# Kernel optimization log

Hardware: AMD Instinct MI355X
Metric: run time of the kernel (lower is better)

## Reference

```python
import jax, jax.numpy as jnp
import numpy as np

N_NODES = 100000
N_EDGES = 1600000
IN_F = 256
OUT_F = 128


def setup_inputs() -> dict:
    key = jax.random.key(0)
    k1, k2, k3, k4, k5, k6 = jax.random.split(key, 6)
    init_range = float(np.sqrt(6.0 / (IN_F + OUT_F)))
    stdv = 1.0 / float(np.sqrt(OUT_F))
    return {
        "x": jax.random.normal(k1, (N_NODES, IN_F), dtype=jnp.float32),
        "weight": jax.random.uniform(k2, (IN_F, OUT_F), dtype=jnp.float32, minval=-init_range, maxval=init_range),
        "bias": jax.random.uniform(k3, (OUT_F,), dtype=jnp.float32, minval=-stdv, maxval=stdv),
        "adj_val": jax.random.uniform(k4, (N_EDGES,), dtype=jnp.float32),
        "adj_row": jax.random.randint(k5, (N_EDGES,), 0, N_NODES),  # destination node per edge
        "adj_col": jax.random.randint(k6, (N_EDGES,), 0, N_NODES),  # source node per edge
    }


def reference(x, weight, bias, adj_val, adj_row, adj_col):
    # support = X @ W   (dense GEMM, [N, in] x [in, out])
    support = x @ weight
    # output = spmm(adj, support): gather source rows, scale by edge value,
    # segment-sum into destination rows. Honors COO sparsity; no [N,N] dense.
    gathered = support[adj_col] * adj_val[:, None]          # [E, out]
    out = jax.ops.segment_sum(gathered, adj_row, num_segments=N_NODES)
    return out + bias
```

## Files before the change

kernel.cpp:

```cpp
#include <hip/hip_runtime.h>

#define N_NODES 100000
#define N_EDGES 1600000
#define IN_F 256
#define OUT_F 128

#define NBUCK 1563
#define FBUCK 64
#define CAP 1664

#define SORT_CHUNKS 128
#define CHUNK_E (N_EDGES / SORT_CHUNKS)

#define GEMM_BM 128
#define GEMM_BLOCKS ((N_NODES + GEMM_BM - 1) / GEMM_BM)

typedef __attribute__((ext_vector_type(8))) short bf16x8;
typedef __attribute__((ext_vector_type(4))) float f32x4;

__device__ __forceinline__ unsigned short f2bf(float f) {
    unsigned u = __float_as_uint(f);
    unsigned r = u + 0x7fffu + ((u >> 16) & 1u);
    return (unsigned short)(r >> 16);
}

__global__ __launch_bounds__(256) void wz_kernel(const float* __restrict__ w,
                                                 unsigned short* __restrict__ wt,
                                                 int* __restrict__ cursor) {
    const int tid = threadIdx.x;
    if (blockIdx.x < 128) {
        int c = blockIdx.x;
        wt[c * IN_F + tid] = f2bf(w[tid * OUT_F + c]);
    } else {
        int i = (blockIdx.x - 128) * 256 + tid;
        if (i < NBUCK) cursor[i] = 0;
    }
}

__global__ __launch_bounds__(512, 4) void gemm_sort_kernel(const float* __restrict__ x,
                                                           const unsigned short* __restrict__ wt,
                                                           unsigned short* __restrict__ support,
                                                           const int* __restrict__ rowi,
                                                           const int* __restrict__ coli,
                                                           const float* __restrict__ val,
                                                           int* __restrict__ cursor,
                                                           uint2* __restrict__ tmp) {
    __shared__ unsigned short ws[128 * 256];
    __shared__ int bh[NBUCK];

    const int tid = threadIdx.x;

    if (blockIdx.x < SORT_CHUNKS) {
        const int c = blockIdx.x;
        for (int i = tid; i < NBUCK; i += 512) bh[i] = 0;
        __syncthreads();
        const int e0 = c * CHUNK_E;
        for (int i = tid; i < CHUNK_E; i += 512)
            atomicAdd(&bh[rowi[e0 + i] >> 6], 1);
        __syncthreads();
        for (int i = tid; i < NBUCK; i += 512) {
            int n = bh[i];
            bh[i] = n ? atomicAdd(&cursor[i], n) : 0;
        }
        __syncthreads();
        for (int i = tid; i < CHUNK_E; i += 512) {
            int e = e0 + i;
            int dst = rowi[e];
            int b = dst >> 6;
            int pos = atomicAdd(&bh[b], 1);
            tmp[(size_t)b * CAP + pos] =
                make_uint2(((unsigned)(dst & 63) << 17) | (unsigned)coli[e],
                           __float_as_uint(val[e]));
        }
        return;
    }

    const int lane = tid & 63;
    const int wv = tid >> 6;
    const int row0 = (blockIdx.x - SORT_CHUNKS) * GEMM_BM;
    const int l15 = lane & 15;
    const int kq = lane >> 4;

#pragma unroll
    for (int it = 0; it < 8; ++it) {
        int ci = it * 512 + tid;
        int col = ci >> 5, ch = ci & 31;
        uint4 v = *reinterpret_cast<const uint4*>(&wt[col * IN_F + ch * 8]);
        int slot = ch ^ (col & 7);
        *reinterpret_cast<uint4*>(&ws[col * 256 + slot * 8]) = v;
    }
    __syncthreads();

    int arow = row0 + wv * 16 + l15;
    if (arow > N_NODES - 1) arow = N_NODES - 1;
    const float* xrow = &x[(size_t)arow * IN_F + kq * 8];

    f32x4 acc[8];
#pragma unroll
    for (int n = 0; n < 8; ++n) acc[n] = (f32x4){0.f, 0.f, 0.f, 0.f};

#pragma unroll
    for (int kt = 0; kt < 8; ++kt) {
        f32x4 a0 = *reinterpret_cast<const f32x4*>(xrow + kt * 32);
        f32x4 a1 = *reinterpret_cast<const f32x4*>(xrow + kt * 32 + 4);
        bf16x8 af;
        af[0] = (short)f2bf(a0[0]); af[1] = (short)f2bf(a0[1]);
        af[2] = (short)f2bf(a0[2]); af[3] = (short)f2bf(a0[3]);
        af[4] = (short)f2bf(a1[0]); af[5] = (short)f2bf(a1[1]);
        af[6] = (short)f2bf(a1[2]); af[7] = (short)f2bf(a1[3]);
#pragma unroll
        for (int n = 0; n < 8; ++n) {
            int col = n * 16 + l15;
            int slot = (kt * 4 + kq) ^ (col & 7);
            bf16x8 bfv = *reinterpret_cast<const bf16x8*>(&ws[col * 256 + slot * 8]);
            acc[n] = __builtin_amdgcn_mfma_f32_16x16x32_bf16(af, bfv, acc[n], 0, 0, 0);
        }
    }

#pragma unroll
    for (int r = 0; r < 4; ++r) {
        int row = row0 + wv * 16 + kq * 4 + r;
        if (row < N_NODES) {
#pragma unroll
            for (int n = 0; n < 8; ++n) {
                support[(size_t)row * OUT_F + n * 16 + l15] = f2bf(acc[n][r]);
            }
        }
    }
}

__global__ __launch_bounds__(256) void fine_accum_kernel(const unsigned short* __restrict__ support,
                                                         const uint2* __restrict__ tmp,
                                                         const int* __restrict__ cursor,
                                                         const float* __restrict__ bias,
                                                         float* __restrict__ out) {
    __shared__ uint2 plds[CAP];
    __shared__ int hist[FBUCK];
    __shared__ int scanb[FBUCK];
    __shared__ int cur[FBUCK];

    const int tid = threadIdx.x, b = blockIdx.x;
    const int cnt = cursor[b];
    const size_t base = (size_t)b * CAP;

    if (tid < FBUCK) hist[tid] = 0;
    __syncthreads();
    for (int i = tid; i < cnt; i += 256)
        atomicAdd(&hist[tmp[base + i].x >> 17], 1);
    __syncthreads();
    if (tid < FBUCK) scanb[tid] = hist[tid];
    __syncthreads();
#pragma unroll
    for (int off = 1; off < FBUCK; off <<= 1) {
        int t = (tid < FBUCK && tid >= off) ? scanb[tid - off] : 0;
        __syncthreads();
        if (tid < FBUCK) scanb[tid] += t;
        __syncthreads();
    }
    if (tid < FBUCK) cur[tid] = scanb[tid] - hist[tid];
    __syncthreads();
    for (int i = tid; i < cnt; i += 256) {
        uint2 u = tmp[base + i];
        int dl = u.x >> 17;
        int pos = atomicAdd(&cur[dl], 1);
        plds[pos] = make_uint2(u.x & 0x1FFFFu, u.y);
    }
    __syncthreads();

    const int lane = tid & 63;
    const int wv = tid >> 6;
    const int grp = lane >> 4;
    const int l16 = lane & 15;

    float4 b0 = *reinterpret_cast<const float4*>(&bias[l16 * 8]);
    float4 b1 = *reinterpret_cast<const float4*>(&bias[l16 * 8 + 4]);

    for (int ni = 0; ni < 16; ++ni) {
        const int dl = wv * 16 + ni;
        const int node = b * FBUCK + dl;
        if (node >= N_NODES) break;
        const int s = (dl == 0) ? 0 : scanb[dl - 1];
        const int e = scanb[dl];

        float acc[8];
#pragma unroll
        for (int t = 0; t < 8; ++t) acc[t] = 0.f;

        int j = s + grp;
        for (; j + 4 < e; j += 8) {
            uint2 p0 = plds[j];
            uint2 p1 = plds[j + 4];
            uint4 s0 = *reinterpret_cast<const uint4*>(&support[(size_t)p0.x * OUT_F + l16 * 8]);
            uint4 s1 = *reinterpret_cast<const uint4*>(&support[(size_t)p1.x * OUT_F + l16 * 8]);
            float v0 = __uint_as_float(p0.y);
            float v1 = __uint_as_float(p1.y);
            unsigned u0[4] = {s0.x, s0.y, s0.z, s0.w};
            unsigned u1[4] = {s1.x, s1.y, s1.z, s1.w};
#pragma unroll
            for (int q = 0; q < 4; ++q) {
                acc[2 * q + 0] += __uint_as_float(u0[q] << 16) * v0;
                acc[2 * q + 1] += __uint_as_float(u0[q] & 0xffff0000u) * v0;
                acc[2 * q + 0] += __uint_as_float(u1[q] << 16) * v1;
                acc[2 * q + 1] += __uint_as_float(u1[q] & 0xffff0000u) * v1;
            }
        }
        for (; j < e; j += 4) {
            uint2 p0 = plds[j];
            uint4 s0 = *reinterpret_cast<const uint4*>(&support[(size_t)p0.x * OUT_F + l16 * 8]);
            float v0 = __uint_as_float(p0.y);
            unsigned u0[4] = {s0.x, s0.y, s0.z, s0.w};
#pragma unroll
            for (int q = 0; q < 4; ++q) {
                acc[2 * q + 0] += __uint_as_float(u0[q] << 16) * v0;
                acc[2 * q + 1] += __uint_as_float(u0[q] & 0xffff0000u) * v0;
            }
        }

#pragma unroll
        for (int t = 0; t < 8; ++t) {
            acc[t] += __shfl_xor(acc[t], 16);
            acc[t] += __shfl_xor(acc[t], 32);
        }

        if (grp == 0) {
            f32x4 o0 = {acc[0] + b0.x, acc[1] + b0.y, acc[2] + b0.z, acc[3] + b0.w};
            f32x4 o1 = {acc[4] + b1.x, acc[5] + b1.y, acc[6] + b1.z, acc[7] + b1.w};
            f32x4* op = reinterpret_cast<f32x4*>(&out[(size_t)node * OUT_F + l16 * 8]);
            __builtin_nontemporal_store(o0, op);
            __builtin_nontemporal_store(o1, op + 1);
        }
    }
}

extern "C" void kernel_launch(void* const* d_in, const int* in_sizes, int n_in,
                              void* d_out, int out_size, void* d_ws, size_t ws_size,
                              hipStream_t stream) {
    const float* x       = (const float*)d_in[0];
    const float* weight  = (const float*)d_in[1];
    const float* bias    = (const float*)d_in[2];
    const float* adj_val = (const float*)d_in[3];
    const int*   adj_row = (const int*)d_in[4];
    const int*   adj_col = (const int*)d_in[5];
    float* out = (float*)d_out;

    unsigned short* support = (unsigned short*)d_ws;
    unsigned short* wt = support + (size_t)N_NODES * OUT_F;
    int* cursor = (int*)(wt + IN_F * OUT_F);
    uint2* tmp = (uint2*)(cursor + 1564);

    wz_kernel<<<128 + 7, 256, 0, stream>>>(weight, wt, cursor);
    gemm_sort_kernel<<<SORT_CHUNKS + GEMM_BLOCKS, 512, 0, stream>>>(
        x, wt, support, adj_row, adj_col, adj_val, cursor, tmp);
    fine_accum_kernel<<<NBUCK, 256, 0, stream>>>(support, tmp, cursor, bias, out);
}
```

Measured before the change: 116.1 us.

## Move edge bucket counting into the first kernel, scatter alongside GEMM

Splits the two-pass bucket sort across kernels. The histogram and the per-chunk bucket base reservation now run in the first kernel, together with the weight transpose, and write per-chunk bases to a workspace table. The GEMM kernel's sort blocks then only scatter edges, so the sort blocks sharing the GEMM launch are shorter and should not delay it. The sort chunk count also doubles to 256, and cursor zeroing moves to a memset. This costs an extra kernel/memset launch, a bases table of about 1.6 MB, and a second read of the row indices.

```diff
diff --git a/kernel.cpp b/kernel.cpp
--- a/kernel.cpp
+++ b/kernel.cpp
@@ -9,8 +9,8 @@
 #define FBUCK 64
 #define CAP 1664
 
-#define SORT_CHUNKS 128
-#define CHUNK_E (N_EDGES / SORT_CHUNKS)
+#define NCHUNK 256
+#define CHUNK_E (N_EDGES / NCHUNK)
 
 #define GEMM_BM 128
 #define GEMM_BLOCKS ((N_NODES + GEMM_BM - 1) / GEMM_BM)
@@ -24,50 +24,55 @@
     return (unsigned short)(r >> 16);
 }
 
-__global__ __launch_bounds__(256) void wz_kernel(const float* __restrict__ w,
-                                                 unsigned short* __restrict__ wt,
-                                                 int* __restrict__ cursor) {
+__global__ __launch_bounds__(256) void count_wtrans_kernel(const int* __restrict__ rowi,
+                                                           int* __restrict__ cursor,
+                                                           int* __restrict__ bases,
+                                                           const float* __restrict__ w,
+                                                           unsigned short* __restrict__ wt) {
     const int tid = threadIdx.x;
-    if (blockIdx.x < 128) {
-        int c = blockIdx.x;
+    if (blockIdx.x >= NCHUNK) {
+        int c = blockIdx.x - NCHUNK;
         wt[c * IN_F + tid] = f2bf(w[tid * OUT_F + c]);
-    } else {
-        int i = (blockIdx.x - 128) * 256 + tid;
-        if (i < NBUCK) cursor[i] = 0;
-    }
-}
-
-__global__ __launch_bounds__(512, 4) void gemm_sort_kernel(const float* __restrict__ x,
-                                                           const unsigned short* __restrict__ wt,
-                                                           unsigned short* __restrict__ support,
-                                                           const int* __restrict__ rowi,
-                                                           const int* __restrict__ coli,
-                                                           const float* __restrict__ val,
-                                                           int* __restrict__ cursor,
-                                                           uint2* __restrict__ tmp) {
+        return;
+    }
+    __shared__ int bh[NBUCK];
+    const int c = blockIdx.x;
+    for (int i = tid; i < NBUCK; i += 256) bh[i] = 0;
+    __syncthreads();
+    const int e0 = c * CHUNK_E;
+    for (int i = tid; i < CHUNK_E; i += 256)
+        atomicAdd(&bh[rowi[e0 + i] >> 6], 1);
+    __syncthreads();
+    for (int i = tid; i < NBUCK; i += 256) {
+        int n = bh[i];
+        bases[i * NCHUNK + c] = n ? atomicAdd(&cursor[i], n) : 0;
+    }
+}
+
+__global__ __launch_bounds__(512, 4) void gemm_scatter_kernel(const float* __restrict__ x,
+                                                              const unsigned short* __restrict__ wt,
+                                                              unsigned short* __restrict__ support,
+                                                              const int* __restrict__ rowi,
+                                                              const int* __restrict__ coli,
+                                                              const float* __restrict__ val,
+                                                              const int* __restrict__ bases,
+                                                              uint2* __restrict__ tmp) {
     __shared__ unsigned short ws[128 * 256];
-    __shared__ int bh[NBUCK];
+    __shared__ int cur[NBUCK];
 
     const int tid = threadIdx.x;
 
-    if (blockIdx.x < SORT_CHUNKS) {
+    if (blockIdx.x < NCHUNK) {
         const int c = blockIdx.x;
-        for (int i = tid; i < NBUCK; i += 512) bh[i] = 0;
+        for (int i = tid; i < NBUCK; i += 512)
+            cur[i] = bases[i * NCHUNK + c];
         __syncthreads();
         const int e0 = c * CHUNK_E;
-        for (int i = tid; i < CHUNK_E; i += 512)
-            atomicAdd(&bh[rowi[e0 + i] >> 6], 1);
-        __syncthreads();
-        for (int i = tid; i < NBUCK; i += 512) {
-            int n = bh[i];
-            bh[i] = n ? atomicAdd(&cursor[i], n) : 0;
-        }
-        __syncthreads();
         for (int i = tid; i < CHUNK_E; i += 512) {
             int e = e0 + i;
             int dst = rowi[e];
             int b = dst >> 6;
-            int pos = atomicAdd(&bh[b], 1);
+            int pos = atomicAdd(&cur[b], 1);
             tmp[(size_t)b * CAP + pos] =
                 make_uint2(((unsigned)(dst & 63) << 17) | (unsigned)coli[e],
                            __float_as_uint(val[e]));
@@ -77,7 +82,7 @@
 
     const int lane = tid & 63;
     const int wv = tid >> 6;
-    const int row0 = (blockIdx.x - SORT_CHUNKS) * GEMM_BM;
+    const int row0 = (blockIdx.x - NCHUNK) * GEMM_BM;
     const int l15 = lane & 15;
     const int kq = lane >> 4;
 
@@ -246,10 +251,12 @@
     unsigned short* support = (unsigned short*)d_ws;
     unsigned short* wt = support + (size_t)N_NODES * OUT_F;
     int* cursor = (int*)(wt + IN_F * OUT_F);
-    uint2* tmp = (uint2*)(cursor + 1564);
-
-    wz_kernel<<<128 + 7, 256, 0, stream>>>(weight, wt, cursor);
-    gemm_sort_kernel<<<SORT_CHUNKS + GEMM_BLOCKS, 512, 0, stream>>>(
-        x, wt, support, adj_row, adj_col, adj_val, cursor, tmp);
+    int* bases = cursor + 1564;
+    uint2* tmp = (uint2*)(bases + NBUCK * NCHUNK);
+
+    hipMemsetAsync(cursor, 0, NBUCK * sizeof(int), stream);
+    count_wtrans_kernel<<<NCHUNK + 128, 256, 0, stream>>>(adj_row, cursor, bases, weight, wt);
+    gemm_scatter_kernel<<<NCHUNK + GEMM_BLOCKS, 512, 0, stream>>>(
+        x, wt, support, adj_row, adj_col, adj_val, bases, tmp);
     fine_accum_kernel<<<NBUCK, 256, 0, stream>>>(support, tmp, cursor, bias, out);
 }
```

Result: slower. 138.2 us (+19.1%).
